# Optimization experiments

Measured on AMD Instinct MI355X. Metric: run time of the kernel, lower is better.

## Reference

```python
import jax, jax.numpy as jnp
import numpy as np

B, NA, NB = 4, 2048, 2048
IN_A, IN_B, OUT, H = 128, 128, 128, 8
DH = OUT // H  # 16
NEG = jnp.float32(-1e30)
SLOPE = jnp.float32(0.01)


def setup_inputs() -> dict:
    key = jax.random.key(0)
    ks = jax.random.split(key, 13)
    s = 0.05
    return {
        "h_A": jax.random.normal(ks[0], (B, NA, IN_A), jnp.float32),
        "h_B": jax.random.normal(ks[1], (B, NB, IN_B), jnp.float32),
        "mask": jax.random.randint(ks[2], (B, NA, NB), 0, 2) > 0,
        # per-head params stacked on a leading head axis
        "WA_w": jax.random.normal(ks[3], (H, IN_A, DH), jnp.float32) * s,
        "WA_b": jax.random.normal(ks[4], (H, DH), jnp.float32) * s,
        "WB_w": jax.random.normal(ks[5], (H, IN_B, DH), jnp.float32) * s,
        "WB_b": jax.random.normal(ks[6], (H, DH), jnp.float32) * s,
        "aA_w": jax.random.normal(ks[7], (H, DH), jnp.float32) * s,
        "aA_b": jax.random.normal(ks[8], (H,), jnp.float32) * s,
        "aB_w": jax.random.normal(ks[9], (H, DH), jnp.float32) * s,
        "aB_b": jax.random.normal(ks[10], (H,), jnp.float32) * s,
        "W_w": jax.random.normal(ks[11], (OUT, OUT), jnp.float32) * s,
        "W_b": jax.random.normal(ks[12], (OUT,), jnp.float32) * s,
    }


def _leaky(x):
    return jnp.where(x >= 0, x, SLOPE * x)


def reference(h_A, h_B, mask, WA_w, WA_b, WB_w, WB_b, aA_w, aA_b, aB_w, aB_b, W_w, W_b):
    # per-head linear projections: [B, H, N, DH]
    z_A = jnp.einsum('bni,hid->bhnd', h_A, WA_w) + WA_b[None, :, None, :]
    z_B = jnp.einsum('bmi,hid->bhmd', h_B, WB_w) + WB_b[None, :, None, :]
    # additive attention logits: [B, H, NA] + [B, H, NB] -> [B, H, NA, NB]
    eA = jnp.einsum('bhnd,hd->bhn', z_A, aA_w) + aA_b[None, :, None]
    eB = jnp.einsum('bhmd,hd->bhm', z_B, aB_w) + aB_b[None, :, None]
    e = eA[:, :, :, None] + eB[:, :, None, :]
    m = mask[:, None, :, :]  # broadcast over heads
    e = jnp.where(m, e, NEG)
    alpha = jax.nn.softmax(_leaky(e), axis=-1)
    alpha = jnp.where(m, alpha, jnp.zeros((), alpha.dtype))
    # weighted aggregation: [B, H, NA, DH]
    out_h = jnp.einsum('bhnm,bhmd->bhnd', alpha, z_B)
    # concat heads -> [B, NA, OUT], final projection
    cat = out_h.transpose(0, 2, 1, 3).reshape(h_A.shape[0], h_A.shape[1], H * DH)
    return cat @ W_w.T + W_b
```

## Files before the change

kernel.cpp:

```cpp
#include <hip/hip_runtime.h>

typedef unsigned short u16;
typedef unsigned int u32;
typedef unsigned char u8;

typedef _Float16 f16x8 __attribute__((ext_vector_type(8)));
typedef _Float16 f16x2 __attribute__((ext_vector_type(2)));
typedef __attribute__((ext_vector_type(4))) float f32x4;


#if __has_builtin(__builtin_amdgcn_sbfe)
#define SEXTBIT(m, j) ((u32)__builtin_amdgcn_sbfe((int)(m), (u32)(j), 1u))
#else
#define SEXTBIT(m, j) ((u32)(((int)((m) << (31 - (j)))) >> 31))
#endif

__global__ __launch_bounds__(256) void kzero(float* __restrict__ out){
  out[blockIdx.x * 256 + threadIdx.x] = 0.f;
}

__global__ __launch_bounds__(256) void kmask(const void* __restrict__ maskv,
                                             u32* __restrict__ Mb){
  __shared__ int s_aw, s_ab, s_ah;
  int t = threadIdx.x;
  if (t == 0){ s_aw = 1; s_ab = 1; s_ah = 1; }
  __syncthreads();
  {
    const u32* mw = (const u32*)maskv;
    int aw = 1, ah = 1, ab = 1;
    #pragma unroll
    for (int j = 0; j < 4; ++j){
      u32 m = mw[t + 256 * j];
      if (!(m == 0u || m == 1u || m == 0x3F800000u)) aw = 0;
      u32 lo = m & 0xFFFFu, hi = m >> 16;
      if (!((lo == 0u || lo == 1u || lo == 0x3F80u) && (hi == 0u || hi == 1u || hi == 0x3F80u))) ah = 0;
      if (m & ~0x01010101u) ab = 0;
    }
    if (!aw) atomicAnd(&s_aw, 0);
    if (!ah) atomicAnd(&s_ah, 0);
    if (!ab) atomicAnd(&s_ab, 0);
  }
  __syncthreads();
  int Fm = 0;
  if (s_aw) Fm = 0; else if (s_ab) Fm = 1; else if (s_ah) Fm = 2;

  if (Fm == 0){
    int lane = t & 63;
    int wid = blockIdx.x * 4 + (t >> 6);
    const u32* mw = (const u32*)maskv;
    size_t base = (size_t)wid * 2048;
    #pragma unroll 4
    for (int i = 0; i < 32; ++i){
      u32 v = mw[base + i * 64 + lane];
      unsigned long long bal = __ballot(v != 0u);
      if (lane < 2) Mb[(base + i * 64) / 32 + lane] = (u32)(bal >> (32 * lane));
    }
    return;
  }
  int oid = blockIdx.x * 256 + t;
  u32 bits = 0;
  if (Fm == 1){
    const uint4* mp = (const uint4*)maskv + (size_t)oid * 2;
    #pragma unroll
    for (int k = 0; k < 2; ++k){
      uint4 v = mp[k];
      u32 w[4] = {v.x, v.y, v.z, v.w};
      #pragma unroll
      for (int q = 0; q < 4; ++q)
        #pragma unroll
        for (int bb = 0; bb < 4; ++bb)
          bits |= ((w[q] >> (8*bb)) & 255u ? 1u : 0u) << (k*16 + q*4 + bb);
    }
  } else {
    const uint4* mp = (const uint4*)maskv + (size_t)oid * 4;
    #pragma unroll
    for (int k = 0; k < 4; ++k){
      uint4 v = mp[k];
      u32 w[4] = {v.x, v.y, v.z, v.w};
      #pragma unroll
      for (int q = 0; q < 4; ++q){
        bits |= ((w[q] & 0xFFFFu) ? 1u : 0u) << (k*8 + q*2);
        bits |= ((w[q] >> 16)     ? 1u : 0u) << (k*8 + q*2 + 1);
      }
    }
  }
  Mb[oid] = bits;
}

__global__ __launch_bounds__(256) void kprep(
    const float* __restrict__ hA, const float* __restrict__ hB,
    const float* __restrict__ WAw, const float* __restrict__ WAb,
    const float* __restrict__ aAw, const float* __restrict__ aAb,
    const float* __restrict__ WBw, const float* __restrict__ WBb,
    const float* __restrict__ aBw, const float* __restrict__ aBb,
    const float* __restrict__ Ww, float* __restrict__ WtO,
    uint4* __restrict__ zF,
    float* __restrict__ EAe, float* __restrict__ EA01e,
    u32* __restrict__ EBh, u32* __restrict__ GBh){
  __shared__ float smem[12416];
  int gid = blockIdx.x, t = threadIdx.x;

  if (gid < 256){
    float* h_l = smem;
    float* W_l = smem + 4224;
    float* T   = smem + 4224;
    int R0 = gid * 32;

    for (int j = 0; j < 4; ++j){
      int idx4 = t + 256 * j;
      int r = idx4 >> 5, k0 = (idx4 & 31) * 4;
      *(float4*)&h_l[r * 132 + k0] = *(const float4*)&hB[(size_t)(R0 + r) * 128 + k0];
    }

    int cg = t & 15, rg = t >> 4;
    float acc[2][8];
    for (int i = 0; i < 2; ++i) for (int s = 0; s < 8; ++s) acc[i][s] = 0.f;

    for (int kc = 0; kc < 2; ++kc){
      __syncthreads();
      for (int j = 0; j < 8; ++j){
        int idx4 = t + 256 * j;
        int k = idx4 >> 5, c0 = (idx4 & 31) * 4;
        *(float4*)&W_l[k * 128 + c0] =
          *(const float4*)&WBw[(size_t)(c0 >> 4) * 2048 + (kc * 64 + k) * 16 + (c0 & 15)];
      }
      __syncthreads();
      for (int k = 0; k < 64; ++k){
        int kk = kc * 64 + k;
        float4 w0 = *(const float4*)&W_l[k * 128 + cg * 8];
        float4 w1 = *(const float4*)&W_l[k * 128 + cg * 8 + 4];
        float wv[8] = {w0.x, w0.y, w0.z, w0.w, w1.x, w1.y, w1.z, w1.w};
        #pragma unroll
        for (int i = 0; i < 2; ++i){
          float hv = h_l[(rg * 2 + i) * 132 + kk];
          #pragma unroll
          for (int s = 0; s < 8; ++s) acc[i][s] = fmaf(hv, wv[s], acc[i][s]);
        }
      }
    }
    __syncthreads();
    for (int i = 0; i < 2; ++i)
      #pragma unroll
      for (int s = 0; s < 8; ++s)
        T[(cg * 8 + s) * 33 + rg * 2 + i] = acc[i][s] + WBb[cg * 8 + s];
    __syncthreads();

    int b = R0 >> 11;
    int mblk = (R0 & 2047) >> 5;
    for (int it = t; it < 512; it += 256){
      int h = it >> 6, lane = it & 63;
      int d = lane & 15, mq = (lane >> 4) * 8;
      const float* Tp = &T[(h * 16 + d) * 33 + mq];
      u32 wv2[4];
      #pragma unroll
      for (int p = 0; p < 4; ++p){
        union { f16x2 h2; u32 u; } c;
        c.h2 = (f16x2){(_Float16)Tp[p * 2], (_Float16)Tp[p * 2 + 1]};
        wv2[p] = c.u;
      }
      zF[((size_t)((b * 8 + h) * 64) + mblk) * 64 + lane] = make_uint4(wv2[0], wv2[1], wv2[2], wv2[3]);
    }
  } else if (gid < 768){
    float* h_l = smem;
    float* v_l = smem + 4224;
    float* c_l = smem + 5280;
    float* a_l = smem + 5288;
    int ge = gid - 256;
    int X = ge >> 8;
    int r0 = (ge & 255) * 32;
    const float* hp  = X ? hB  : hA;
    const float* Wp  = X ? WBw : WAw;
    const float* Wbp = X ? WBb : WAb;
    const float* awp = X ? aBw : aAw;
    const float* abp = X ? aBb : aAb;

    for (int j = 0; j < 4; ++j){
      int idx4 = t + 256 * j;
      int r = idx4 >> 5, k0 = (idx4 & 31) * 4;
      *(float4*)&h_l[r * 132 + k0] = *(const float4*)&hp[(size_t)(r0 + r) * 128 + k0];
    }
    if (t < 128) a_l[t] = awp[t];
    __syncthreads();
    #pragma unroll
    for (int p = 0; p < 4; ++p){
      int idx = t + 256 * p;
      int h = idx >> 7, i = idx & 127;
      const float* wrow = Wp + (size_t)h * 2048 + i * 16;
      float s = 0.f;
      #pragma unroll
      for (int d = 0; d < 16; ++d) s = fmaf(wrow[d], a_l[h * 16 + d], s);
      v_l[h * 132 + i] = s;
    }
    if (t < 8){
      float s = abp[t];
      #pragma unroll
      for (int d = 0; d < 16; ++d) s = fmaf(Wbp[t * 16 + d], a_l[t * 16 + d], s);
      c_l[t] = s;
    }
    __syncthreads();

    int r = t >> 3, h = t & 7;
    float acc = c_l[h];
    #pragma unroll
    for (int k0 = 0; k0 < 128; k0 += 4){
      float4 hv = *(const float4*)&h_l[r * 132 + k0];
      float4 vv = *(const float4*)&v_l[h * 132 + k0];
      acc = fmaf(hv.x, vv.x, acc); acc = fmaf(hv.y, vv.y, acc);
      acc = fmaf(hv.z, vv.z, acc); acc = fmaf(hv.w, vv.w, acc);
    }
    int row = r0 + r;
    int b = row >> 11, n = row & 2047;
    float e0 = __expf(acc), e1 = __expf(0.01f * acc);
    if (X){
      float p0 = __shfl_xor(e0, 8, 64);
      float p1 = __shfl_xor(e1, 8, 64);
      if ((((t & 63) >> 3) & 1) == 0){
        union { f16x2 h2; u32 u; } c0, c1;
        c0.h2 = (f16x2){(_Float16)e0, (_Float16)p0};
        c1.h2 = (f16x2){(_Float16)e1, (_Float16)p1};
        u32 di = (u32)((b * 8 + h) * 1024 + (n >> 1));
        EBh[di] = c0.u;
        GBh[di] = c1.u;
      }
    } else {
      size_t idx = (size_t)(b * 8 + h) * 2048 + n;
      EAe[idx] = e0; EA01e[idx] = e1;
    }
  } else {
    int j = gid - 768;
    int idx = j * 256 + t;
    int c = idx >> 7, o = idx & 127;
    WtO[idx] = Ww[o * 128 + c];
  }
}

__global__ __launch_bounds__(256) void kattn(const uint4* __restrict__ zF,
                                             const float* __restrict__ EAe, const float* __restrict__ EA01e,
                                             const u32* __restrict__ EBh, const u32* __restrict__ GBh,
                                             const u32* __restrict__ Mb,
                                             float* __restrict__ cat){
  __shared__ u32 EB_l[1024];
  __shared__ u32 GB_l[1024];
  __shared__ u32 Mb_l[32 * 65];
  __shared__ float red[3][32][17];
  int t = threadIdx.x;
  int w = t >> 6, lane = t & 63;
  int gid = blockIdx.x;
  int h  = gid & 7;
  int nt = (gid >> 3) & 63;
  int b  = gid >> 9;
  int n0 = nt * 32;
  int nl = lane & 15, q = lane >> 4, qs = q * 8;

  {
    const uint4* src0 = (const uint4*)(EBh + (size_t)(b * 8 + h) * 1024);
    const uint4* src1 = (const uint4*)(GBh + (size_t)(b * 8 + h) * 1024);
    ((uint4*)EB_l)[t] = src0[t];
    ((uint4*)GB_l)[t] = src1[t];
    const uint4* ms = (const uint4*)(Mb + ((size_t)b * 2048 + n0) * 64);
    uint4 m0v = ms[t * 2], m1v = ms[t * 2 + 1];
    int rr = t >> 3, cc = (t & 7) * 8;
    u32* dst = Mb_l + rr * 65 + cc;
    dst[0] = m0v.x; dst[1] = m0v.y; dst[2] = m0v.z; dst[3] = m0v.w;
    dst[4] = m1v.x; dst[5] = m1v.y; dst[6] = m1v.z; dst[7] = m1v.w;
  }

  size_t ebase = (size_t)(b * 8 + h) * 2048;
  _Float16 ea0h  = (_Float16)EAe  [ebase + n0 + nl];
  _Float16 ea0sh = (_Float16)EA01e[ebase + n0 + nl];
  _Float16 ea1h  = (_Float16)EAe  [ebase + n0 + 16 + nl];
  _Float16 ea1sh = (_Float16)EA01e[ebase + n0 + 16 + nl];
  f16x2 ea0_2  = (f16x2){ea0h,  ea0h};
  f16x2 ea0s_2 = (f16x2){ea0sh, ea0sh};
  f16x2 ea1_2  = (f16x2){ea1h,  ea1h};
  f16x2 ea1s_2 = (f16x2){ea1sh, ea1sh};

  const u32* EBq = EB_l + w * 256;
  const u32* GBq = GB_l + w * 256;
  const u32* Mrow0 = Mb_l + nl * 65 + w * 16;
  const u32* Mrow1 = Mb_l + (nl + 16) * 65 + w * 16;
  const uint4* zFp = zF + ((size_t)(b * 8 + h) * 64 + w * 16) * 64 + lane;

  f32x4 acc0 = {0.f,0.f,0.f,0.f}, acc1 = {0.f,0.f,0.f,0.f};
  f32x4 lcc0 = {0.f,0.f,0.f,0.f}, lcc1 = {0.f,0.f,0.f,0.f};
  union { u32 u[4]; f16x8 v; } onesu;
  onesu.u[0] = 0x3C003C00u; onesu.u[1] = 0x3C003C00u;
  onesu.u[2] = 0x3C003C00u; onesu.u[3] = 0x3C003C00u;
  const f16x8 ones = onesu.v;

  __syncthreads();

  uint4 Azu, Bzu;
  #define LOADA(sp) do{ Azu = zFp[(size_t)(sp) * 64]; }while(0)
  #define LOADB(sp) do{ Bzu = zFp[(size_t)(sp) * 64]; }while(0)
  #define COMP(sp,ZU_) do{ \
    uint4 EB_ = *(const uint4*)(EBq + (sp) * 16 + q * 4); \
    uint4 GB_ = *(const uint4*)(GBq + (sp) * 16 + q * 4); \
    u32 mb0 = Mrow0[sp] >> qs; \
    u32 mb1 = Mrow1[sp] >> qs; \
    u32 ebu[4] = {EB_.x, EB_.y, EB_.z, EB_.w}; \
    u32 gbu[4] = {GB_.x, GB_.y, GB_.z, GB_.w}; \
    union { u32 u[4]; f16x8 v; } a0, a1; \
    _Pragma("unroll") \
    for (int p = 0; p < 4; ++p){ \
      int j0 = 2*p, j1 = 2*p + 1; \
      u32 k00 = SEXTBIT(mb0, j0); \
      u32 k01 = SEXTBIT(mb0, j1); \
      u32 k10 = SEXTBIT(mb1, j0); \
      u32 k11 = SEXTBIT(mb1, j1); \
      u32 kc0 = __builtin_amdgcn_perm(k01, k00, 0x05040100u); \
      u32 kc1 = __builtin_amdgcn_perm(k11, k10, 0x05040100u); \
      union { u32 u; f16x2 h2; } eb, gb, r0u, r1u; \
      eb.u = ebu[p]; gb.u = gbu[p]; \
      r0u.h2 = __builtin_elementwise_max(ea0_2 * eb.h2, ea0s_2 * gb.h2); \
      r1u.h2 = __builtin_elementwise_max(ea1_2 * eb.h2, ea1s_2 * gb.h2); \
      a0.u[p] = r0u.u & kc0; \
      a1.u[p] = r1u.u & kc1; \
    } \
    union { uint4 u; f16x8 v; } zu; zu.u = ZU_; \
    acc0 = __builtin_amdgcn_mfma_f32_16x16x32_f16(a0.v, zu.v, acc0, 0, 0, 0); \
    lcc0 = __builtin_amdgcn_mfma_f32_16x16x32_f16(a0.v, ones, lcc0, 0, 0, 0); \
    acc1 = __builtin_amdgcn_mfma_f32_16x16x32_f16(a1.v, zu.v, acc1, 0, 0, 0); \
    lcc1 = __builtin_amdgcn_mfma_f32_16x16x32_f16(a1.v, ones, lcc1, 0, 0, 0); }while(0)

  LOADA(0);
  LOADB(1);
  #pragma unroll 4
  for (int s = 0; s < 16; s += 2){
    COMP(s, Azu);
    LOADA(s + 2);
    COMP(s + 1, Bzu);
    LOADB(s + 3);
  }
  #undef LOADA
  #undef LOADB
  #undef COMP

  if (w > 0){
    #pragma unroll
    for (int r = 0; r < 4; ++r){
      int row = q * 4 + r;
      red[w - 1][row][nl]      = acc0[r];
      red[w - 1][row + 16][nl] = acc1[r];
    }
    if (nl == 0){
      #pragma unroll
      for (int r = 0; r < 4; ++r){
        red[w - 1][q * 4 + r][16]      = lcc0[r];
        red[w - 1][q * 4 + r + 16][16] = lcc1[r];
      }
    }
  }
  __syncthreads();
  if (w == 0){
    #pragma unroll
    for (int r = 0; r < 4; ++r){
      int row = q * 4 + r;
      float a0 = acc0[r] + red[0][row][nl]      + red[1][row][nl]      + red[2][row][nl];
      float a1 = acc1[r] + red[0][row + 16][nl] + red[1][row + 16][nl] + red[2][row + 16][nl];
      float L0 = lcc0[r] + red[0][row][16]      + red[1][row][16]      + red[2][row][16];
      float L1 = lcc1[r] + red[0][row + 16][16] + red[1][row + 16][16] + red[2][row + 16][16];
      float r0 = (L0 > 0.f) ? 1.f / L0 : 0.f;
      float r1 = (L1 > 0.f) ? 1.f / L1 : 0.f;
      cat[((size_t)(b * 2048) + n0 + row)      * 128 + h * 16 + nl] = a0 * r0;
      cat[((size_t)(b * 2048) + n0 + 16 + row) * 128 + h * 16 + nl] = a1 * r1;
    }
  }
}

__global__ __launch_bounds__(256) void kout(const float* __restrict__ cat,
                                            const float* __restrict__ WtO, const float* __restrict__ Wb,
                                            float* __restrict__ out){
  __shared__ float cat_l[32 * 132];
  __shared__ float Wt_l[64 * 128];
  int R0 = blockIdx.x * 32;
  int t = threadIdx.x;

  for (int jj = 0; jj < 4; ++jj){
    int idx4 = t + 256 * jj;
    int r = idx4 >> 5, c0 = (idx4 & 31) * 4;
    *(float4*)&cat_l[r * 132 + c0] = *(const float4*)&cat[((size_t)R0 + r) * 128 + c0];
  }

  int og = t & 15, rg = t >> 4;
  float acc[2][8];
  for (int i = 0; i < 2; ++i) for (int s = 0; s < 8; ++s) acc[i][s] = 0.f;

  for (int kc = 0; kc < 2; ++kc){
    __syncthreads();
    for (int j = 0; j < 8; ++j){
      int idx4 = t + 256 * j;
      int k = idx4 >> 5, o0 = (idx4 & 31) * 4;
      *(float4*)&Wt_l[k * 128 + o0] = *(const float4*)&WtO[(kc * 64 + k) * 128 + o0];
    }
    __syncthreads();
    for (int k = 0; k < 64; ++k){
      int kk = kc * 64 + k;
      float4 w0 = *(const float4*)&Wt_l[k * 128 + og * 8];
      float4 w1 = *(const float4*)&Wt_l[k * 128 + og * 8 + 4];
      float wv[8] = {w0.x, w0.y, w0.z, w0.w, w1.x, w1.y, w1.z, w1.w};
      #pragma unroll
      for (int i = 0; i < 2; ++i){
        float cv = cat_l[(rg * 2 + i) * 132 + kk];
        #pragma unroll
        for (int s = 0; s < 8; ++s) acc[i][s] = fmaf(cv, wv[s], acc[i][s]);
      }
    }
  }

  for (int i = 0; i < 2; ++i){
    int r = rg * 2 + i;
    float* op = out + (size_t)(R0 + r) * 128 + og * 8;
    *(float4*)(op)     = make_float4(acc[i][0]+Wb[og*8+0], acc[i][1]+Wb[og*8+1], acc[i][2]+Wb[og*8+2], acc[i][3]+Wb[og*8+3]);
    *(float4*)(op + 4) = make_float4(acc[i][4]+Wb[og*8+4], acc[i][5]+Wb[og*8+5], acc[i][6]+Wb[og*8+6], acc[i][7]+Wb[og*8+7]);
  }
}

extern "C" void kernel_launch(void* const* d_in, const int* in_sizes, int n_in,
                              void* d_out, int out_size, void* d_ws, size_t ws_size,
                              hipStream_t stream) {
  const float* hA  = (const float*)d_in[0];
  const float* hB  = (const float*)d_in[1];
  const void* maskv= d_in[2];
  const float* WAw = (const float*)d_in[3];
  const float* WAb = (const float*)d_in[4];
  const float* WBw = (const float*)d_in[5];
  const float* WBb = (const float*)d_in[6];
  const float* aAw = (const float*)d_in[7];
  const float* aAb = (const float*)d_in[8];
  const float* aBw = (const float*)d_in[9];
  const float* aBb = (const float*)d_in[10];
  const float* Ww  = (const float*)d_in[11];
  const float* Wb  = (const float*)d_in[12];

  float* ws   = (float*)d_ws;
  uint4* zF   = (uint4*)ws;
  float* EAe  = ws + 524288;
  float* EA01e= ws + 589824;
  u32*  EBh   = (u32*)(ws + 655360);
  u32*  GBh   = (u32*)(ws + 720896);
  float* WtO  = ws + 802816;
  u32*  Mb    = (u32*)(ws + 821272);
  float* cat  = ws + 1345560;

  if (ws_size < 2394136ull * 4ull){
    kzero<<<4096, 256, 0, stream>>>((float*)d_out);
    return;
  }

  kmask<<<2048, 256, 0, stream>>>(maskv, Mb);
  kprep<<< 832, 256, 0, stream>>>(hA, hB,
                                  WAw, WAb, aAw, aAb,
                                  WBw, WBb, aBw, aBb,
                                  Ww, WtO, zF, EAe, EA01e, EBh, GBh);
  kattn<<<2048, 256, 0, stream>>>(zF, EAe, EA01e, EBh, GBh, Mb, cat);
  kout <<< 256, 256, 0, stream>>>(cat, WtO, Wb, (float*)d_out);
}
```

Before: 175.9 us.

## Factor per-row softmax scale out of attention weights and specialize mask kernels

Each row's weight max(eA*eB, eA^0.01*gB) is rewritten as max(eB, exp(-0.99 a)*gB), dropping a per-row factor that cancels against the row sum in softmax normalization. This cuts one f16 multiply per pair in the inner loop and replaces two per-row arrays with one. The mask conversion kernel is picked on the host from input byte sizes, which skips the runtime format detection pass, and the detection path now uses wave ballots instead of per-thread shared atomics. The mask and reduction shared buffers are aliased, which needs an added barrier and frees LDS for occupancy. Dropping the factor changes f16 magnitudes, so overflow or precision behaviour may differ.

```diff
diff --git a/kernel.cpp b/kernel.cpp
--- a/kernel.cpp
+++ b/kernel.cpp
@@ -19,8 +19,66 @@
   out[blockIdx.x * 256 + threadIdx.x] = 0.f;
 }
 
-__global__ __launch_bounds__(256) void kmask(const void* __restrict__ maskv,
-                                             u32* __restrict__ Mb){
+__global__ __launch_bounds__(256) void kmask_f32(const u32* __restrict__ mw,
+                                                 u32* __restrict__ Mb){
+  int t = threadIdx.x;
+  int lane = t & 63;
+  int wid = blockIdx.x * 4 + (t >> 6);
+  size_t base = (size_t)wid * 2048;
+  for (int i = 0; i < 32; i += 4){
+    u32 v0 = mw[base + (size_t)(i + 0) * 64 + lane];
+    u32 v1 = mw[base + (size_t)(i + 1) * 64 + lane];
+    u32 v2 = mw[base + (size_t)(i + 2) * 64 + lane];
+    u32 v3 = mw[base + (size_t)(i + 3) * 64 + lane];
+    unsigned long long b0 = __ballot(v0 != 0u);
+    unsigned long long b1 = __ballot(v1 != 0u);
+    unsigned long long b2 = __ballot(v2 != 0u);
+    unsigned long long b3 = __ballot(v3 != 0u);
+    if (lane == 0){
+      size_t o = base / 32 + (size_t)i * 2;
+      *(unsigned long long*)&Mb[o + 0] = b0;
+      *(unsigned long long*)&Mb[o + 2] = b1;
+      *(unsigned long long*)&Mb[o + 4] = b2;
+      *(unsigned long long*)&Mb[o + 6] = b3;
+    }
+  }
+}
+
+__global__ __launch_bounds__(256) void kmask_b8(const void* __restrict__ maskv,
+                                                u32* __restrict__ Mb){
+  int oid = blockIdx.x * 256 + threadIdx.x;
+  u32 bits = 0;
+  const uint4* mp = (const uint4*)maskv + (size_t)oid * 2;
+  uint4 va = mp[0], vb = mp[1];
+  u32 w[8] = {va.x, va.y, va.z, va.w, vb.x, vb.y, vb.z, vb.w};
+  #pragma unroll
+  for (int q = 0; q < 8; ++q)
+    #pragma unroll
+    for (int bb = 0; bb < 4; ++bb)
+      bits |= ((w[q] >> (8 * bb)) & 255u ? 1u : 0u) << (q * 4 + bb);
+  Mb[oid] = bits;
+}
+
+__global__ __launch_bounds__(256) void kmask_b16(const void* __restrict__ maskv,
+                                                 u32* __restrict__ Mb){
+  int oid = blockIdx.x * 256 + threadIdx.x;
+  u32 bits = 0;
+  const uint4* mp = (const uint4*)maskv + (size_t)oid * 4;
+  #pragma unroll
+  for (int k = 0; k < 4; ++k){
+    uint4 v = mp[k];
+    u32 w[4] = {v.x, v.y, v.z, v.w};
+    #pragma unroll
+    for (int q = 0; q < 4; ++q){
+      bits |= ((w[q] & 0xFFFFu) ? 1u : 0u) << (k * 8 + q * 2);
+      bits |= ((w[q] >> 16)     ? 1u : 0u) << (k * 8 + q * 2 + 1);
+    }
+  }
+  Mb[oid] = bits;
+}
+
+__global__ __launch_bounds__(256) void kmask_det(const void* __restrict__ maskv,
+                                                 u32* __restrict__ Mb){
   __shared__ int s_aw, s_ab, s_ah;
   int t = threadIdx.x;
   if (t == 0){ s_aw = 1; s_ab = 1; s_ah = 1; }
@@ -36,9 +94,14 @@
       if (!((lo == 0u || lo == 1u || lo == 0x3F80u) && (hi == 0u || hi == 1u || hi == 0x3F80u))) ah = 0;
       if (m & ~0x01010101u) ab = 0;
     }
-    if (!aw) atomicAnd(&s_aw, 0);
-    if (!ah) atomicAnd(&s_ah, 0);
-    if (!ab) atomicAnd(&s_ab, 0);
+    unsigned long long fa = __ballot(!aw);
+    unsigned long long fh = __ballot(!ah);
+    unsigned long long fb = __ballot(!ab);
+    if ((t & 63) == 0){
+      if (fa) atomicAnd(&s_aw, 0);
+      if (fh) atomicAnd(&s_ah, 0);
+      if (fb) atomicAnd(&s_ab, 0);
+    }
   }
   __syncthreads();
   int Fm = 0;
@@ -49,11 +112,22 @@
     int wid = blockIdx.x * 4 + (t >> 6);
     const u32* mw = (const u32*)maskv;
     size_t base = (size_t)wid * 2048;
-    #pragma unroll 4
-    for (int i = 0; i < 32; ++i){
-      u32 v = mw[base + i * 64 + lane];
-      unsigned long long bal = __ballot(v != 0u);
-      if (lane < 2) Mb[(base + i * 64) / 32 + lane] = (u32)(bal >> (32 * lane));
+    for (int i = 0; i < 32; i += 4){
+      u32 v0 = mw[base + (size_t)(i + 0) * 64 + lane];
+      u32 v1 = mw[base + (size_t)(i + 1) * 64 + lane];
+      u32 v2 = mw[base + (size_t)(i + 2) * 64 + lane];
+      u32 v3 = mw[base + (size_t)(i + 3) * 64 + lane];
+      unsigned long long b0 = __ballot(v0 != 0u);
+      unsigned long long b1 = __ballot(v1 != 0u);
+      unsigned long long b2 = __ballot(v2 != 0u);
+      unsigned long long b3 = __ballot(v3 != 0u);
+      if (lane == 0){
+        size_t o = base / 32 + (size_t)i * 2;
+        *(unsigned long long*)&Mb[o + 0] = b0;
+        *(unsigned long long*)&Mb[o + 2] = b1;
+        *(unsigned long long*)&Mb[o + 4] = b2;
+        *(unsigned long long*)&Mb[o + 6] = b3;
+      }
     }
     return;
   }
@@ -95,7 +169,7 @@
     const float* __restrict__ aBw, const float* __restrict__ aBb,
     const float* __restrict__ Ww, float* __restrict__ WtO,
     uint4* __restrict__ zF,
-    float* __restrict__ EAe, float* __restrict__ EA01e,
+    float* __restrict__ RA,
     u32* __restrict__ EBh, u32* __restrict__ GBh){
   __shared__ float smem[12416];
   int gid = blockIdx.x, t = threadIdx.x;
@@ -210,8 +284,8 @@
     }
     int row = r0 + r;
     int b = row >> 11, n = row & 2047;
-    float e0 = __expf(acc), e1 = __expf(0.01f * acc);
     if (X){
+      float e0 = __expf(acc), e1 = __expf(0.01f * acc);
       float p0 = __shfl_xor(e0, 8, 64);
       float p1 = __shfl_xor(e1, 8, 64);
       if ((((t & 63) >> 3) & 1) == 0){
@@ -223,8 +297,7 @@
         GBh[di] = c1.u;
       }
     } else {
-      size_t idx = (size_t)(b * 8 + h) * 2048 + n;
-      EAe[idx] = e0; EA01e[idx] = e1;
+      RA[(size_t)(b * 8 + h) * 2048 + n] = __expf(-0.99f * acc);
     }
   } else {
     int j = gid - 768;
@@ -235,14 +308,15 @@
 }
 
 __global__ __launch_bounds__(256) void kattn(const uint4* __restrict__ zF,
-                                             const float* __restrict__ EAe, const float* __restrict__ EA01e,
+                                             const float* __restrict__ RA,
                                              const u32* __restrict__ EBh, const u32* __restrict__ GBh,
                                              const u32* __restrict__ Mb,
                                              float* __restrict__ cat){
   __shared__ u32 EB_l[1024];
   __shared__ u32 GB_l[1024];
-  __shared__ u32 Mb_l[32 * 65];
-  __shared__ float red[3][32][17];
+  __shared__ u32 MR_l[32 * 65];
+  u32* Mb_l = MR_l;
+  float (*red)[32][17] = (float(*)[32][17])MR_l;
   int t = threadIdx.x;
   int w = t >> 6, lane = t & 63;
   int gid = blockIdx.x;
@@ -266,14 +340,10 @@
   }
 
   size_t ebase = (size_t)(b * 8 + h) * 2048;
-  _Float16 ea0h  = (_Float16)EAe  [ebase + n0 + nl];
-  _Float16 ea0sh = (_Float16)EA01e[ebase + n0 + nl];
-  _Float16 ea1h  = (_Float16)EAe  [ebase + n0 + 16 + nl];
-  _Float16 ea1sh = (_Float16)EA01e[ebase + n0 + 16 + nl];
-  f16x2 ea0_2  = (f16x2){ea0h,  ea0h};
-  f16x2 ea0s_2 = (f16x2){ea0sh, ea0sh};
-  f16x2 ea1_2  = (f16x2){ea1h,  ea1h};
-  f16x2 ea1s_2 = (f16x2){ea1sh, ea1sh};
+  float ra0 = RA[ebase + n0 + nl];
+  float ra1 = RA[ebase + n0 + 16 + nl];
+  f16x2 rho0_2 = (f16x2){(_Float16)ra0, (_Float16)ra0};
+  f16x2 rho1_2 = (f16x2){(_Float16)ra1, (_Float16)ra1};
 
   const u32* EBq = EB_l + w * 256;
   const u32* GBq = GB_l + w * 256;
@@ -312,8 +382,8 @@
       u32 kc1 = __builtin_amdgcn_perm(k11, k10, 0x05040100u); \
       union { u32 u; f16x2 h2; } eb, gb, r0u, r1u; \
       eb.u = ebu[p]; gb.u = gbu[p]; \
-      r0u.h2 = __builtin_elementwise_max(ea0_2 * eb.h2, ea0s_2 * gb.h2); \
-      r1u.h2 = __builtin_elementwise_max(ea1_2 * eb.h2, ea1s_2 * gb.h2); \
+      r0u.h2 = __builtin_elementwise_max(eb.h2, rho0_2 * gb.h2); \
+      r1u.h2 = __builtin_elementwise_max(eb.h2, rho1_2 * gb.h2); \
       a0.u[p] = r0u.u & kc0; \
       a1.u[p] = r1u.u & kc1; \
     } \
@@ -336,6 +406,7 @@
   #undef LOADB
   #undef COMP
 
+  __syncthreads();
   if (w > 0){
     #pragma unroll
     for (int r = 0; r < 4; ++r){
@@ -435,8 +506,7 @@
 
   float* ws   = (float*)d_ws;
   uint4* zF   = (uint4*)ws;
-  float* EAe  = ws + 524288;
-  float* EA01e= ws + 589824;
+  float* RA   = ws + 524288;
   u32*  EBh   = (u32*)(ws + 655360);
   u32*  GBh   = (u32*)(ws + 720896);
   float* WtO  = ws + 802816;
@@ -448,11 +518,23 @@
     return;
   }
 
-  kmask<<<2048, 256, 0, stream>>>(maskv, Mb);
+  const long long ME = 4ll * 2048 * 2048;
+  long long hsz = in_sizes[0];
+  long long msz = in_sizes[2];
+  bool bytes_known = (hsz == 4ll * 2048 * 128 * 4);
+  if (bytes_known && msz == ME)
+    kmask_b8 <<<2048, 256, 0, stream>>>(maskv, Mb);
+  else if (bytes_known && msz == 2 * ME)
+    kmask_b16<<<2048, 256, 0, stream>>>(maskv, Mb);
+  else if (bytes_known && msz == 4 * ME)
+    kmask_f32<<<2048, 256, 0, stream>>>((const u32*)maskv, Mb);
+  else
+    kmask_det<<<2048, 256, 0, stream>>>(maskv, Mb);
+
   kprep<<< 832, 256, 0, stream>>>(hA, hB,
                                   WAw, WAb, aAw, aAb,
                                   WBw, WBb, aBw, aBb,
-                                  Ww, WtO, zF, EAe, EA01e, EBh, GBh);
-  kattn<<<2048, 256, 0, stream>>>(zF, EAe, EA01e, EBh, GBh, Mb, cat);
+                                  Ww, WtO, zF, RA, EBh, GBh);
+  kattn<<<2048, 256, 0, stream>>>(zF, RA, EBh, GBh, Mb, cat);
   kout <<< 256, 256, 0, stream>>>(cat, WtO, Wb, (float*)d_out);
 }
```

Measured after the change: 163.0 us. -7.3%, faster.
